# Kernel tuning notes

Measured on AMD Instinct MI355X. Metric: run time of the kernel, lower is better.

Reference implementation:

```python
import jax, jax.numpy as jnp
import numpy as np

BATCH = 4096
DIM = 512
NOISE_POWER = 1.0


def setup_inputs() -> dict:
    key = jax.random.key(0)
    k1, k2 = jax.random.split(key)
    info = jax.random.normal(k1, (BATCH, DIM), dtype=jnp.float32)
    codewords = jax.random.normal(k2, (BATCH, DIM), dtype=jnp.float32)
    sigma = (NOISE_POWER * jnp.eye(DIM, dtype=jnp.float32))
    return {"info": info, "codewords": codewords, "sigma": sigma}


def _gmm_entropy_upper(mu, sigma):
    """Kolchinsky-style upper bound on Gaussian-mixture entropy.

    Faithful to tensor_entropy_gauss_mix_upper: pairwise Mahalanobis
    quadratic form exponent[i, j] = -0.5 * (mu_i - mu_j)^T Sig^-1 (mu_i - mu_j),
    computed via the Gram-matrix expansion instead of materializing the
    [B*B, dim] repeat/tile intermediates.
    """
    B, dim = mu.shape
    sig_inv = jnp.linalg.inv(sigma)
    A = mu @ sig_inv                      # [B, dim]
    q = jnp.sum(A * mu, axis=1)           # [B] diagonal quadratic terms
    G = A @ mu.T                          # [B, B]  mu_i Sig^-1 mu_j^T
    # expo[i, j] = -0.5*(q_i + q_j - G[i,j] - G[j,i])
    expo = -0.5 * (q[:, None] + q[None, :] - G - G.T)
    lse = jax.nn.logsumexp(expo, axis=1)  # [B], over mixture components j
    weight = 1.0 / B
    factor_log = -(dim / 2.0) * jnp.log(2.0 * jnp.pi * sigma[0, 0])
    log_inner = jnp.log(weight) + factor_log + lse
    entropy = dim / 2.0 - jnp.sum(weight * log_inner)
    return entropy


def reference(info, codewords, sigma):
    # Original call: info, codewords = inputs; info_codewords = codewords
    # (info is unpacked but unused). h_z and h_zm both use codewords.
    h_z = _gmm_entropy_upper(codewords, sigma)
    h_zm = _gmm_entropy_upper(codewords, sigma)
    return jnp.stack([h_z, h_zm])
```

## Files before the change

kernel.cpp:

```cpp
#include <hip/hip_runtime.h>
#include <math.h>

#define NB 4096
#define ND 512
#define TILE 128
#define BK 32
#define NEPOCH 8

typedef __bf16 bf16x8 __attribute__((ext_vector_type(8)));
typedef float floatx4 __attribute__((ext_vector_type(4)));

__device__ inline void async_load16(const void* g, void* l) {
    __builtin_amdgcn_global_load_lds((const __attribute__((address_space(1))) void*)g,
                                     (__attribute__((address_space(3))) void*)l, 16, 0, 0);
}

__global__ __launch_bounds__(256) void prep_kernel(const float* __restrict__ mu,
                                                   __bf16* __restrict__ mubf,
                                                   float* __restrict__ hq,
                                                   float* __restrict__ sumexp) {
    const int t = threadIdx.x;
    const int wave = t >> 6, lane = t & 63;
    const int row = blockIdx.x * 4 + wave;
    const float4* src = (const float4*)(mu + (size_t)row * ND) + lane * 2;
    const float4 v0 = src[0], v1 = src[1];
    bf16x8 pack;
    pack[0] = (__bf16)v0.x; pack[1] = (__bf16)v0.y;
    pack[2] = (__bf16)v0.z; pack[3] = (__bf16)v0.w;
    pack[4] = (__bf16)v1.x; pack[5] = (__bf16)v1.y;
    pack[6] = (__bf16)v1.z; pack[7] = (__bf16)v1.w;
    __builtin_nontemporal_store(pack, (bf16x8*)(mubf + (size_t)row * ND) + lane);
    float sq = 0.0f;
    #pragma unroll
    for (int e = 0; e < 8; e++) { float f = (float)pack[e]; sq += f * f; }
    #pragma unroll
    for (int off = 32; off > 0; off >>= 1) sq += __shfl_down(sq, off, 64);
    if (lane == 0) {
        hq[row] = 0.5f * sq;
        sumexp[row] = 0.0f;
    }
}

__global__ __launch_bounds__(256) void gram_lse_kernel(const __bf16* __restrict__ mubf,
                                                       const float* __restrict__ hq,
                                                       const float* __restrict__ sigma,
                                                       float* __restrict__ sumexp) {
    __shared__ alignas(16) __bf16 As[2][TILE * BK];
    __shared__ alignas(16) __bf16 Bs[2][TILE * BK];

    const int t = threadIdx.x;
    const int row0 = blockIdx.y * TILE;
    const int col0 = blockIdx.x * TILE;
    const int wave = t >> 6;
    const int lane = t & 63;
    const int r16 = lane & 15;
    const int quad = lane >> 4;
    const int rw = (wave >> 1) * 64;
    const int cw = (wave & 1) * 64;

    const int srow = t >> 2;
    const int skoff = (t & 3) * 8;
    const __bf16* gA0 = mubf + (size_t)(row0 + srow) * ND + skoff;
    const __bf16* gA1 = gA0 + (size_t)64 * ND;
    const __bf16* gB0 = mubf + (size_t)(col0 + srow) * ND + skoff;
    const __bf16* gB1 = gB0 + (size_t)64 * ND;

    floatx4 acc[4][4];
    #pragma unroll
    for (int i = 0; i < 4; i++)
        #pragma unroll
        for (int j = 0; j < 4; j++) {
            floatx4 z = {0.f, 0.f, 0.f, 0.f};
            acc[i][j] = z;
        }

    for (int ep = 0; ep < NEPOCH; ep++) {
        const int k0 = ep * 64;
        __syncthreads();
        #pragma unroll
        for (int s = 0; s < 2; s++) {
            const int ks = k0 + s * BK;
            async_load16(gA0 + ks, &As[s][t * 8]);
            async_load16(gA1 + ks, &As[s][2048 + t * 8]);
            async_load16(gB0 + ks, &Bs[s][t * 8]);
            async_load16(gB1 + ks, &Bs[s][2048 + t * 8]);
        }
        __syncthreads();

        #pragma unroll
        for (int s = 0; s < 2; s++) {
            bf16x8 a[4], b[4];
            #pragma unroll
            for (int i = 0; i < 4; i++)
                a[i] = *(const bf16x8*)&As[s][(rw + i * 16 + r16) * BK + quad * 8];
            #pragma unroll
            for (int j = 0; j < 4; j++)
                b[j] = *(const bf16x8*)&Bs[s][(cw + j * 16 + r16) * BK + quad * 8];
            #pragma unroll
            for (int i = 0; i < 4; i++)
                #pragma unroll
                for (int j = 0; j < 4; j++)
                    acc[i][j] = __builtin_amdgcn_mfma_f32_16x16x32_bf16(a[i], b[j], acc[i][j], 0, 0, 0);
        }
    }

    const float inv_s = 1.0f / sigma[0];
    float hqc[4];
    #pragma unroll
    for (int j = 0; j < 4; j++) hqc[j] = hq[col0 + cw + j * 16 + r16];

    #pragma unroll
    for (int i = 0; i < 4; i++) {
        #pragma unroll
        for (int r = 0; r < 4; r++) {
            const int row = row0 + rw + i * 16 + quad * 4 + r;
            const float hr = hq[row];
            float rs = 0.0f;
            #pragma unroll
            for (int j = 0; j < 4; j++)
                rs += __expf((acc[i][j][r] - hr - hqc[j]) * inv_s);
            rs += __shfl_xor(rs, 1, 64);
            rs += __shfl_xor(rs, 2, 64);
            rs += __shfl_xor(rs, 4, 64);
            rs += __shfl_xor(rs, 8, 64);
            if (r16 == 0) atomicAdd(&sumexp[row], rs);
        }
    }
}

__global__ __launch_bounds__(1024) void finalize_kernel(const float* __restrict__ sumexp,
                                                        const float* __restrict__ sigma,
                                                        float* __restrict__ out) {
    const int t = threadIdx.x;
    float local = 0.0f;
    for (int i = t; i < NB; i += 1024) local += logf(sumexp[i]);
    #pragma unroll
    for (int off = 32; off > 0; off >>= 1) local += __shfl_down(local, off, 64);
    __shared__ float red[16];
    if ((t & 63) == 0) red[t >> 6] = local;
    __syncthreads();
    if (t == 0) {
        double tot = 0.0;
        #pragma unroll
        for (int i = 0; i < 16; i++) tot += (double)red[i];
        const double s = (double)sigma[0];
        const double ent = (double)(ND / 2)
                         + log((double)NB)
                         + (double)(ND / 2) * log(2.0 * M_PI * s)
                         - tot / (double)NB;
        out[0] = (float)ent;
        out[1] = (float)ent;
    }
}

extern "C" void kernel_launch(void* const* d_in, const int* in_sizes, int n_in,
                              void* d_out, int out_size, void* d_ws, size_t ws_size,
                              hipStream_t stream) {
    (void)in_sizes; (void)n_in; (void)out_size; (void)ws_size;
    const float* codewords = (const float*)d_in[1];
    const float* sigma     = (const float*)d_in[2];
    float* out = (float*)d_out;

    char* ws = (char*)d_ws;
    __bf16* mubf   = (__bf16*)ws;
    float*  hq     = (float*)(ws + (size_t)NB * ND * 2);
    float*  sumexp = hq + NB;

    prep_kernel<<<NB / 4, 256, 0, stream>>>(codewords, mubf, hq, sumexp);
    dim3 grid(NB / TILE, NB / TILE);
    gram_lse_kernel<<<grid, 256, 0, stream>>>(mubf, hq, sigma, sumexp);
    finalize_kernel<<<1, 1024, 0, stream>>>(sumexp, sigma, out);
}
```

Before: 111.8 us.

## Pre-swizzle bf16 data into MFMA fragment layout and load directly to registers

The prep kernel now writes the bf16 copy in a layout grouped by 16-row block and 32-wide k-chunk, so each MFMA lane's fragment is one contiguous 16-byte vector. The gram kernel drops shared memory and barriers, loading fragments straight from global memory into registers with a two-stage register double buffer. This removes LDS staging and __syncthreads, at the cost of redundant global/L2 reads since waves no longer share tiles.

```diff
diff --git a/kernel.cpp b/kernel.cpp
--- a/kernel.cpp
+++ b/kernel.cpp
@@ -4,19 +4,14 @@
 #define NB 4096
 #define ND 512
 #define TILE 128
-#define BK 32
-#define NEPOCH 8
+#define NKC (ND / 32)
 
 typedef __bf16 bf16x8 __attribute__((ext_vector_type(8)));
 typedef float floatx4 __attribute__((ext_vector_type(4)));
 
-__device__ inline void async_load16(const void* g, void* l) {
-    __builtin_amdgcn_global_load_lds((const __attribute__((address_space(1))) void*)g,
-                                     (__attribute__((address_space(3))) void*)l, 16, 0, 0);
-}
 
 __global__ __launch_bounds__(256) void prep_kernel(const float* __restrict__ mu,
-                                                   __bf16* __restrict__ mubf,
+                                                   __bf16* __restrict__ mubf2,
                                                    float* __restrict__ hq,
                                                    float* __restrict__ sumexp) {
     const int t = threadIdx.x;
@@ -29,7 +24,9 @@
     pack[2] = (__bf16)v0.z; pack[3] = (__bf16)v0.w;
     pack[4] = (__bf16)v1.x; pack[5] = (__bf16)v1.y;
     pack[6] = (__bf16)v1.z; pack[7] = (__bf16)v1.w;
-    __builtin_nontemporal_store(pack, (bf16x8*)(mubf + (size_t)row * ND) + lane);
+    const size_t slot = ((size_t)(row >> 4) * NKC + (lane >> 2)) * 64
+                      + (size_t)(lane & 3) * 16 + (row & 15);
+    __builtin_nontemporal_store(pack, (bf16x8*)mubf2 + slot);
     float sq = 0.0f;
     #pragma unroll
     for (int e = 0; e < 8; e++) { float f = (float)pack[e]; sq += f * f; }
@@ -41,29 +38,28 @@
     }
 }
 
-__global__ __launch_bounds__(256) void gram_lse_kernel(const __bf16* __restrict__ mubf,
+__global__ __launch_bounds__(256) void gram_lse_kernel(const __bf16* __restrict__ mubf2,
                                                        const float* __restrict__ hq,
                                                        const float* __restrict__ sigma,
                                                        float* __restrict__ sumexp) {
-    __shared__ alignas(16) __bf16 As[2][TILE * BK];
-    __shared__ alignas(16) __bf16 Bs[2][TILE * BK];
-
     const int t = threadIdx.x;
-    const int row0 = blockIdx.y * TILE;
-    const int col0 = blockIdx.x * TILE;
     const int wave = t >> 6;
     const int lane = t & 63;
     const int r16 = lane & 15;
     const int quad = lane >> 4;
     const int rw = (wave >> 1) * 64;
     const int cw = (wave & 1) * 64;
+    const int row0 = blockIdx.y * TILE + rw;
+    const int col0 = blockIdx.x * TILE + cw;
 
-    const int srow = t >> 2;
-    const int skoff = (t & 3) * 8;
-    const __bf16* gA0 = mubf + (size_t)(row0 + srow) * ND + skoff;
-    const __bf16* gA1 = gA0 + (size_t)64 * ND;
-    const __bf16* gB0 = mubf + (size_t)(col0 + srow) * ND + skoff;
-    const __bf16* gB1 = gB0 + (size_t)64 * ND;
+    const bf16x8* pA[4];
+    const bf16x8* pB[4];
+    #pragma unroll
+    for (int i = 0; i < 4; i++)
+        pA[i] = (const bf16x8*)mubf2 + ((size_t)(row0 / 16 + i) * NKC) * 64 + lane;
+    #pragma unroll
+    for (int j = 0; j < 4; j++)
+        pB[j] = (const bf16x8*)mubf2 + ((size_t)(col0 / 16 + j) * NKC) * 64 + lane;
 
     floatx4 acc[4][4];
     #pragma unroll
@@ -74,46 +70,38 @@
             acc[i][j] = z;
         }
 
-    for (int ep = 0; ep < NEPOCH; ep++) {
-        const int k0 = ep * 64;
-        __syncthreads();
+    bf16x8 fa[2][4], fb[2][4];
+    #pragma unroll
+    for (int i = 0; i < 4; i++) fa[0][i] = pA[i][0];
+    #pragma unroll
+    for (int j = 0; j < 4; j++) fb[0][j] = pB[j][0];
+
+    #pragma unroll
+    for (int kc = 0; kc < NKC; kc++) {
+        const int cur = kc & 1, nxt = cur ^ 1;
+        if (kc < NKC - 1) {
+            #pragma unroll
+            for (int i = 0; i < 4; i++) fa[nxt][i] = pA[i][(kc + 1) * 64];
+            #pragma unroll
+            for (int j = 0; j < 4; j++) fb[nxt][j] = pB[j][(kc + 1) * 64];
+        }
         #pragma unroll
-        for (int s = 0; s < 2; s++) {
-            const int ks = k0 + s * BK;
-            async_load16(gA0 + ks, &As[s][t * 8]);
-            async_load16(gA1 + ks, &As[s][2048 + t * 8]);
-            async_load16(gB0 + ks, &Bs[s][t * 8]);
-            async_load16(gB1 + ks, &Bs[s][2048 + t * 8]);
-        }
-        __syncthreads();
-
-        #pragma unroll
-        for (int s = 0; s < 2; s++) {
-            bf16x8 a[4], b[4];
-            #pragma unroll
-            for (int i = 0; i < 4; i++)
-                a[i] = *(const bf16x8*)&As[s][(rw + i * 16 + r16) * BK + quad * 8];
+        for (int i = 0; i < 4; i++)
             #pragma unroll
             for (int j = 0; j < 4; j++)
-                b[j] = *(const bf16x8*)&Bs[s][(cw + j * 16 + r16) * BK + quad * 8];
-            #pragma unroll
-            for (int i = 0; i < 4; i++)
-                #pragma unroll
-                for (int j = 0; j < 4; j++)
-                    acc[i][j] = __builtin_amdgcn_mfma_f32_16x16x32_bf16(a[i], b[j], acc[i][j], 0, 0, 0);
-        }
+                acc[i][j] = __builtin_amdgcn_mfma_f32_16x16x32_bf16(fa[cur][i], fb[cur][j], acc[i][j], 0, 0, 0);
     }
 
     const float inv_s = 1.0f / sigma[0];
     float hqc[4];
     #pragma unroll
-    for (int j = 0; j < 4; j++) hqc[j] = hq[col0 + cw + j * 16 + r16];
+    for (int j = 0; j < 4; j++) hqc[j] = hq[col0 + j * 16 + r16];
 
     #pragma unroll
     for (int i = 0; i < 4; i++) {
         #pragma unroll
         for (int r = 0; r < 4; r++) {
-            const int row = row0 + rw + i * 16 + quad * 4 + r;
+            const int row = row0 + i * 16 + quad * 4 + r;
             const float hr = hq[row];
             float rs = 0.0f;
             #pragma unroll
@@ -162,12 +150,12 @@
     float* out = (float*)d_out;
 
     char* ws = (char*)d_ws;
-    __bf16* mubf   = (__bf16*)ws;
+    __bf16* mubf2  = (__bf16*)ws;
     float*  hq     = (float*)(ws + (size_t)NB * ND * 2);
     float*  sumexp = hq + NB;
 
-    prep_kernel<<<NB / 4, 256, 0, stream>>>(codewords, mubf, hq, sumexp);
+    prep_kernel<<<NB / 4, 256, 0, stream>>>(codewords, mubf2, hq, sumexp);
     dim3 grid(NB / TILE, NB / TILE);
-    gram_lse_kernel<<<grid, 256, 0, stream>>>(mubf, hq, sigma, sumexp);
+    gram_lse_kernel<<<grid, 256, 0, stream>>>(mubf2, hq, sigma, sumexp);
     finalize_kernel<<<1, 1024, 0, stream>>>(sumexp, sigma, out);
 }
```

New measurement: 121.4 us. 1.09x slower.
